# Kernel optimization log

Measured on AMD Instinct MI355X. Metric: run time of the kernel, lower is better.

## Reference

```python
import jax, jax.numpy as jnp
import numpy as np
import math

H, G, DQK, DV = 16, 4, 64, 128  # n_head, n_kv_group, qk head dim, v head dim


def _rope(t):
    # t: [B, n, T, d] -- standard rotate-half RoPE, base 10000
    B, n, T, d = t.shape
    inv = 1.0 / (10000.0 ** (jnp.arange(0, d, 2, dtype=jnp.float32) / d))  # [d/2]
    ang = jnp.arange(T, dtype=jnp.float32)[:, None] * inv[None, :]          # [T, d/2]
    cos = jnp.concatenate([jnp.cos(ang), jnp.cos(ang)], axis=-1)            # [T, d]
    sin = jnp.concatenate([jnp.sin(ang), jnp.sin(ang)], axis=-1)
    t1, t2 = jnp.split(t, 2, axis=-1)
    rot = jnp.concatenate([-t2, t1], axis=-1)
    return t * cos + rot * sin


def setup_inputs() -> dict:
    key = jax.random.key(0)
    ks = jax.random.split(key, 6)
    B, T, C = 2, 2048, 1024
    x = jax.random.normal(ks[0], (B, T, C), jnp.float32)
    Wq = jax.random.normal(ks[1], (C, H * DQK), jnp.float32) * 0.02
    Wk = jax.random.normal(ks[2], (C, G * DQK), jnp.float32) * 0.02
    Wv = jax.random.normal(ks[3], (C, G * DV), jnp.float32) * 0.02
    Wproj = jax.random.normal(ks[4], (DV, C), jnp.float32) * 0.02
    lobo = jnp.full((H,), 1.0, jnp.float32)  # flash_lobo_log_const per head
    g0 = math.log2(T * T - T)                # qk_norm_factor init from block_size
    qk_norm_factor = jnp.array([g0], dtype=jnp.float32)
    return {"x": x, "iter_num": 0, "Wq": Wq, "Wk": Wk, "Wv": Wv,
            "Wproj": Wproj, "lobo": lobo, "qk_norm_factor": qk_norm_factor}


def reference(x, iter_num, Wq, Wk, Wv, Wproj, lobo, qk_norm_factor):
    B, T, C = x.shape
    # projections (bias=False)
    q = (x @ Wq).reshape(B, T, H, DQK).transpose(0, 2, 1, 3)   # [B,H,T,dqk]
    k = (x @ Wk).reshape(B, T, G, DQK).transpose(0, 2, 1, 3)   # [B,G,T,dqk]
    v = (x @ Wv).reshape(B, T, G, DV).transpose(0, 2, 1, 3)    # [B,G,T,dv]
    # rotary embeddings on q and k
    q = _rope(q)
    k = _rope(k)
    # qk-norm
    q = q / (jnp.linalg.norm(q, axis=-1, keepdims=True) + 1e-6)
    k = k / (jnp.linalg.norm(k, axis=-1, keepdims=True) + 1e-6)
    # learned logit scale: q *= g*sqrt(d), SDPA divides by sqrt(d) -> net scale g
    q = q * (qk_norm_factor[0] * jnp.sqrt(jnp.float32(DQK)))
    # GQA broadcast (repeat_interleave over kv groups)
    rep = H // G
    k = jnp.repeat(k, rep, axis=1)   # [B,H,T,dqk]
    v = jnp.repeat(v, rep, axis=1)   # [B,H,T,dv]
    logits = jnp.einsum('bhqd,bhkd->bhqk', q, k) / jnp.sqrt(jnp.float32(DQK))
    causal = jnp.tril(jnp.ones((T, T), dtype=bool))
    logits = jnp.where(causal[None, None], logits, -jnp.inf)
    # flash-lobo: zero-valued sink key, always visible, logit = per-head bias
    sink = jnp.broadcast_to(lobo[None, :, None, None], (B, H, T, 1))
    att = jax.nn.softmax(jnp.concatenate([sink, logits], axis=-1), axis=-1)
    y = jnp.einsum('bhqk,bhkd->bhqd', att[..., 1:], v)  # sink value is zero
    y = y.sum(axis=1)                                    # head-SUM merge [B,T,dv]
    return y @ Wproj                                     # [B,T,C]
```

## Files before the change

### kernel.cpp

```cpp
#include <hip/hip_runtime.h>
#include <hip/hip_bf16.h>
#include <math.h>

#define B_ 2
#define T_ 2048
#define C_ 1024
#define H_ 16
#define G_ 4
#define DQK_ 64
#define DV_ 128
#define NQKV 1792
#define QKW 1280
#define KS2 2048

typedef __attribute__((ext_vector_type(8))) short short8;
typedef __attribute__((ext_vector_type(4))) float f32x4;
typedef unsigned short ushort_t;

__device__ inline ushort_t f2bf(float f) {
  union { float f; unsigned int u; } v; v.f = f;
  unsigned int r = (v.u + 0x7FFFu + ((v.u >> 16) & 1u)) >> 16;
  return (ushort_t)r;
}
__device__ inline float bf2f(ushort_t h) {
  union { unsigned int u; float f; } v; v.u = ((unsigned int)h) << 16;
  return v.f;
}
__device__ inline ushort_t f2bf_hw(float f) {
  unsigned int u;
  asm("v_cvt_pk_bf16_f32 %0, %1, %1" : "=v"(u) : "v"(f));
  return (ushort_t)u;
}

#define GLD_LDS16(g, l)                                              \
  __builtin_amdgcn_global_load_lds(                                  \
      (const __attribute__((address_space(1))) void*)(g),            \
      (__attribute__((address_space(3))) void*)(l), 16, 0, 0)

__global__ __launch_bounds__(256) void prep(
    const float* __restrict__ x, const float* __restrict__ Wq,
    const float* __restrict__ Wk, const float* __restrict__ Wv,
    const float* __restrict__ Wproj, ushort_t* __restrict__ xb,
    ushort_t* __restrict__ wt, ushort_t* __restrict__ wpf) {
  __shared__ float tile[64][65];
  const int bid = blockIdx.x;
  const int tid = threadIdx.x;

  if (bid < 2048) {
    int idx = bid * 256 + tid;
    int m = idx >> 7;
    int c8 = idx & 127;
    const float* src = &x[(size_t)m * 1024 + c8 * 8];
    float4 v0 = *(const float4*)&src[0];
    float4 v1 = *(const float4*)&src[4];
    float f[8] = {v0.x, v0.y, v0.z, v0.w, v1.x, v1.y, v1.z, v1.w};
    short8 hv, lv;
#pragma unroll
    for (int c = 0; c < 8; c++) {
      ushort_t h = f2bf(f[c]);
      hv[c] = (short)h;
      lv[c] = (short)f2bf(f[c] - bf2f(h));
    }
    int key = (m >> 1) & 3;
    int phys = (c8 & ~3) * 8 + ((c8 & 3) ^ key) * 8;
    ushort_t* row = xb + (size_t)m * KS2;
    *(short8*)&row[phys] = hv;
    *(short8*)&row[1024 + phys] = lv;
  } else if (bid < 2496) {
    const int wid = bid - 2048;
    const int n0 = (wid % 28) * 64;
    const int k0 = (wid / 28) * 64;

    const float* Wp; int ldw, noff;
    if (n0 < 1024)      { Wp = Wq; ldw = 1024; noff = n0; }
    else if (n0 < 1280) { Wp = Wk; ldw = 256;  noff = n0 - 1024; }
    else                { Wp = Wv; ldw = 512;  noff = n0 - 1280; }

#pragma unroll
    for (int it = 0; it < 4; it++) {
      int fi = it * 256 + tid;
      int kk = fi >> 4;
      int nc = (fi & 15) * 4;
      float4 v = *(const float4*)&Wp[(size_t)(k0 + kk) * ldw + noff + nc];
      tile[nc + 0][kk] = v.x; tile[nc + 1][kk] = v.y;
      tile[nc + 2][kk] = v.z; tile[nc + 3][kk] = v.w;
    }
    __syncthreads();
    int nn = tid >> 2, seg = tid & 3;
    int n = n0 + nn;
    int key = (n >> 1) & 3;
    ushort_t* row = wt + (size_t)n * KS2;
#pragma unroll
    for (int j = 0; j < 2; j++) {
      short8 hv;
#pragma unroll
      for (int u = 0; u < 8; u++)
        hv[u] = (short)f2bf(tile[nn][seg * 16 + j * 8 + u]);
      int c8 = (k0 >> 3) + seg * 2 + j;
      int phys = (c8 & ~3) * 8 + ((c8 & 3) ^ key) * 8;
      *(short8*)&row[phys] = hv;
    }
  } else {
    int idx = (bid - 2496) * 256 + tid;
    int n = idx & 1023;
    int kc = idx >> 10;
    short8 v;
#pragma unroll
    for (int j = 0; j < 8; j++)
      v[j] = (short)f2bf(Wproj[(size_t)(kc * 8 + j) * 1024 + n]);
    size_t off = (((size_t)(n >> 7) * 4 + (kc >> 2)) * 8 + ((n >> 4) & 7)) * 512 +
                 ((kc & 3) * 16 + (n & 15)) * 8;
    *(short8*)&wpf[off] = v;
  }
}

__global__ __launch_bounds__(256) void gemm_qkv_mfma(
    const ushort_t* __restrict__ xb, const ushort_t* __restrict__ wt,
    float* __restrict__ qkv, ushort_t* __restrict__ vf) {
  __shared__ ushort_t At[128 * 64];
  __shared__ ushort_t Bt[128 * 64];
  const int tid = threadIdx.x;
  const int wave = tid >> 6, lane = tid & 63;
  const int quad = lane >> 4, l16 = lane & 15;
  const int m0 = blockIdx.y * 128, n0 = blockIdx.x * 128;
  const int wm = (wave & 1) * 64, wn = (wave >> 1) * 64;
  const int key = (l16 >> 1) & 3;
  const int ntiles = (n0 >= 1280) ? 16 : 32;

  f32x4 acc[4][4];
#pragma unroll
  for (int i = 0; i < 4; i++)
#pragma unroll
    for (int j = 0; j < 4; j++) acc[i][j] = (f32x4){0.f, 0.f, 0.f, 0.f};

  const int rA = wave * 32 + (lane >> 3);
  const int cA = (lane & 7) * 8;
  const ushort_t* gA = xb + (size_t)(m0 + rA) * KS2 + cA;
  const ushort_t* gB = wt + (size_t)(n0 + rA) * KS2 + cA;

  for (int kt = 0; kt < ntiles; kt++) {
    const int ca = kt * 64;
    const int cb = (kt < 16 ? kt : kt - 16) * 64;
    __syncthreads();
#pragma unroll
    for (int j = 0; j < 4; j++) {
      GLD_LDS16(gA + ca + (size_t)(8 * j) * KS2, &At[(wave * 32 + 8 * j) * 64]);
      GLD_LDS16(gB + cb + (size_t)(8 * j) * KS2, &Bt[(wave * 32 + 8 * j) * 64]);
    }
    __syncthreads();

#pragma unroll
    for (int s = 0; s < 2; s++) {
      const int off = s * 32 + ((quad ^ key) * 8);
      short8 af[4], bf[4];
#pragma unroll
      for (int i = 0; i < 4; i++)
        af[i] = *(const short8*)&At[(wm + 16 * i + l16) * 64 + off];
#pragma unroll
      for (int j = 0; j < 4; j++)
        bf[j] = *(const short8*)&Bt[(wn + 16 * j + l16) * 64 + off];
#pragma unroll
      for (int i = 0; i < 4; i++)
#pragma unroll
        for (int j = 0; j < 4; j++)
          acc[i][j] = __builtin_amdgcn_mfma_f32_16x16x32_bf16(
              af[i], bf[j], acc[i][j], 0, 0, 0);
    }
  }

  if (n0 >= 1280) {
    const int g = (n0 - 1280) >> 7;
    ushort_t* vg = vf + (size_t)g * 262144;
#pragma unroll
    for (int i = 0; i < 4; i++) {
      int mbase = m0 + wm + 16 * i + quad * 4;
#pragma unroll
      for (int jn = 0; jn < 4; jn++) {
        int nv = (wn >> 4) + jn;
#pragma unroll
        for (int r = 0; r < 4; r++) {
          int m = mbase + r;
          int b = m >> 11, t = m & 2047;
          int tk = t >> 6, ks = (t >> 5) & 1, qd = (t >> 3) & 3, jj = t & 7;
          size_t off = (size_t)b * 4 * 262144 +
                       ((size_t)(tk * 16 + ks * 8 + nv) * 4 + qd) * 128 +
                       l16 * 8 + jj;
          vg[off] = f2bf(acc[i][jn][r]);
        }
      }
    }
  } else {
#pragma unroll
    for (int i = 0; i < 4; i++) {
      int m = m0 + wm + 16 * i + quad * 4;
#pragma unroll
      for (int j = 0; j < 4; j++) {
        int n = n0 + wn + 16 * j + l16;
#pragma unroll
        for (int r = 0; r < 4; r++)
          qkv[(size_t)(m + r) * QKW + n] = acc[i][j][r];
      }
    }
  }
}

__global__ __launch_bounds__(256) void rope_scatter(
    const float* __restrict__ qkv, ushort_t* __restrict__ qf,
    ushort_t* __restrict__ kf, float* __restrict__ y) {
  const int bid = blockIdx.x;
  const int tid = threadIdx.x;

  if (bid < 20480) {
    const int NQ = B_ * T_ * H_;
    int vec = bid * 4 + (tid >> 6);
    int d = tid & 63;

    size_t src; int t, b, isq; ushort_t* dstbase;
    if (vec < NQ) {
      int h = vec % H_; int bt = vec / H_;
      t = bt % T_; b = bt / T_;
      src = (size_t)bt * QKW + h * 64 + d;
      dstbase = qf + (size_t)(b * 16 + h) * 131072;
      isq = 1;
    } else {
      int vk = vec - NQ;
      int g = vk % G_; int bt = vk / G_;
      t = bt % T_; b = bt / T_;
      src = (size_t)bt * QKW + 1024 + g * 64 + d;
      dstbase = kf + (size_t)(b * 4 + g) * 131072;
      isq = 0;
    }
    float val = qkv[src];
    int i = d & 31;
    float inv = exp2f(-(float)i * 0.4152410118074239f);
    float ang = (float)t * inv;
    float sn, cs;
    __sincosf(ang, &sn, &cs);
    float partner = __shfl(val, d ^ 32, 64);
    float r = (d < 32) ? (val * cs - partner * sn) : (val * cs + partner * sn);
    float ss = r * r;
#pragma unroll
    for (int off = 32; off; off >>= 1) ss += __shfl_xor(ss, off, 64);
    r *= 1.0f / (sqrtf(ss) + 1e-6f);

    int kt = t >> 6, tt = t & 63;
    int l16v = tt & 15;
    int ks = d >> 5, quad = (d >> 3) & 3, j = d & 7;
    size_t off2;
    if (isq) {
      int wavei = tt >> 4;
      off2 = ((size_t)(kt * 8 + wavei * 2 + ks) * 4 + quad) * 128 + l16v * 8 + j;
    } else {
      int nt = tt >> 4;
      off2 = ((size_t)(kt * 8 + ks * 4 + nt) * 4 + quad) * 128 + l16v * 8 + j;
    }
    dstbase[off2] = f2bf(r);
  } else {
    int idx = (bid - 20480) * 256 + tid;
    *(float4*)&y[(size_t)idx * 4] = (float4){0.f, 0.f, 0.f, 0.f};
  }
}

__global__ __launch_bounds__(256, 4) void attn(
    const ushort_t* __restrict__ qf, const ushort_t* __restrict__ kf,
    const ushort_t* __restrict__ vf, const float* __restrict__ lobo,
    const float* __restrict__ qknf, float* __restrict__ y) {
  const int f = blockIdx.x;
  const int bh = f & 31;
  const int slot = f >> 5;
  int tq;
  if (slot < 8)       tq = 31 - slot;
  else if (slot < 16) tq = 8 + slot;
  else if (slot < 24) tq = 31 - slot;
  else                tq = slot - 24;
  const int b = bh >> 4;
  const int h = bh & 15;
  const int g = h >> 2;

  __shared__ ushort_t KV[12288];
  __shared__ ushort_t Ps[4 * 1088];

  const int tid = threadIdx.x;
  const int wave = tid >> 6, lane = tid & 63;
  const int quad = lane >> 4, l16 = lane & 15;
  ushort_t* PsW = &Ps[wave * 1088];

  short8 bones;
  {
    short bv = (l16 == 0) ? (short)0x3F80 : (short)0;
#pragma unroll
    for (int j = 0; j < 8; j++) bones[j] = bv;
  }

  const ushort_t* qbase = qf + (size_t)(b * 16 + h) * 131072 + lane * 8;
  short8 aq0 = *(const short8*)&qbase[(size_t)(tq * 8 + wave * 2 + 0) * 512];
  short8 aq1 = *(const short8*)&qbase[(size_t)(tq * 8 + wave * 2 + 1) * 512];

  f32x4 o[9];
#pragma unroll
  for (int nv = 0; nv < 9; nv++) o[nv] = (f32x4){0.f, 0.f, 0.f, 0.f};

  const float gsc = qknf[0];
  const float sinkp = __expf(lobo[h] - gsc);

  const int row = tq * 64 + wave * 16 + quad * 4;

  const ushort_t* kgl = kf + (size_t)(b * 4 + g) * 131072 + lane * 8;
  const ushort_t* vgl = vf + (size_t)(b * 4 + g) * 262144 + lane * 8;

  for (int kt = 0; kt <= tq; kt++) {
    __syncthreads();
    {
      const ushort_t* gk = kgl + (size_t)kt * 4096;
      const ushort_t* gv = vgl + (size_t)kt * 8192;
      GLD_LDS16(gk + (wave * 2 + 0) * 512, &KV[(wave * 2 + 0) * 512]);
      GLD_LDS16(gk + (wave * 2 + 1) * 512, &KV[(wave * 2 + 1) * 512]);
#pragma unroll
      for (int j = 0; j < 4; j++)
        GLD_LDS16(gv + (wave * 4 + j) * 512, &KV[4096 + (wave * 4 + j) * 512]);
    }
    __syncthreads();

    f32x4 s[4];
#pragma unroll
    for (int nt = 0; nt < 4; nt++) s[nt] = (f32x4){0.f, 0.f, 0.f, 0.f};
    {
      short8 kb[4];
#pragma unroll
      for (int u = 0; u < 4; u++)
        kb[u] = *(const short8*)&KV[u * 512 + lane * 8];
      __builtin_amdgcn_s_setprio(1);
#pragma unroll
      for (int nt = 0; nt < 4; nt++)
        s[nt] = __builtin_amdgcn_mfma_f32_16x16x32_bf16(aq0, kb[nt], s[nt], 0, 0, 0);
      __builtin_amdgcn_s_setprio(0);
#pragma unroll
      for (int u = 0; u < 4; u++)
        kb[u] = *(const short8*)&KV[(4 + u) * 512 + lane * 8];
      __builtin_amdgcn_s_setprio(1);
#pragma unroll
      for (int nt = 0; nt < 4; nt++)
        s[nt] = __builtin_amdgcn_mfma_f32_16x16x32_bf16(aq1, kb[nt], s[nt], 0, 0, 0);
      __builtin_amdgcn_s_setprio(0);
    }

    if (kt == tq) {
#pragma unroll
      for (int nt = 0; nt < 4; nt++) {
        int key = kt * 64 + l16 + nt * 16;
#pragma unroll
        for (int r = 0; r < 4; r++) {
          float pv = (key <= row + r) ? __expf(fmaf(s[nt][r], gsc, -gsc)) : 0.f;
          PsW[(quad * 4 + r) * 68 + nt * 16 + l16] = f2bf_hw(pv);
        }
      }
    } else {
#pragma unroll
      for (int nt = 0; nt < 4; nt++)
#pragma unroll
        for (int r = 0; r < 4; r++)
          PsW[(quad * 4 + r) * 68 + nt * 16 + l16] =
              f2bf_hw(__expf(fmaf(s[nt][r], gsc, -gsc)));
    }

    short8 ap0 = *(const short8*)&PsW[l16 * 68 + quad * 8];
    short8 ap1 = *(const short8*)&PsW[l16 * 68 + 32 + quad * 8];
    {
      short8 vb[4];
#pragma unroll
      for (int u = 0; u < 4; u++)
        vb[u] = *(const short8*)&KV[4096 + u * 512 + lane * 8];
      __builtin_amdgcn_s_setprio(1);
#pragma unroll
      for (int nv = 0; nv < 4; nv++)
        o[nv] = __builtin_amdgcn_mfma_f32_16x16x32_bf16(ap0, vb[nv], o[nv], 0, 0, 0);
      __builtin_amdgcn_s_setprio(0);
#pragma unroll
      for (int u = 0; u < 4; u++)
        vb[u] = *(const short8*)&KV[4096 + (4 + u) * 512 + lane * 8];
      __builtin_amdgcn_s_setprio(1);
#pragma unroll
      for (int nv = 0; nv < 4; nv++)
        o[4 + nv] = __builtin_amdgcn_mfma_f32_16x16x32_bf16(ap0, vb[nv], o[4 + nv], 0, 0, 0);
      o[8] = __builtin_amdgcn_mfma_f32_16x16x32_bf16(ap0, bones, o[8], 0, 0, 0);
      o[8] = __builtin_amdgcn_mfma_f32_16x16x32_bf16(ap1, bones, o[8], 0, 0, 0);
      __builtin_amdgcn_s_setprio(0);
#pragma unroll
      for (int u = 0; u < 4; u++)
        vb[u] = *(const short8*)&KV[4096 + (8 + u) * 512 + lane * 8];
      __builtin_amdgcn_s_setprio(1);
#pragma unroll
      for (int nv = 0; nv < 4; nv++)
        o[nv] = __builtin_amdgcn_mfma_f32_16x16x32_bf16(ap1, vb[nv], o[nv], 0, 0, 0);
      __builtin_amdgcn_s_setprio(0);
#pragma unroll
      for (int u = 0; u < 4; u++)
        vb[u] = *(const short8*)&KV[4096 + (12 + u) * 512 + lane * 8];
      __builtin_amdgcn_s_setprio(1);
#pragma unroll
      for (int nv = 0; nv < 4; nv++)
        o[4 + nv] = __builtin_amdgcn_mfma_f32_16x16x32_bf16(ap1, vb[nv], o[4 + nv], 0, 0, 0);
      __builtin_amdgcn_s_setprio(0);
    }
  }

#pragma unroll
  for (int r = 0; r < 4; r++) {
    float lm = __shfl(o[8][r], lane & 48, 64);
    float invl = 1.0f / (lm + sinkp);
    size_t gRow = (size_t)b * T_ + row + r;
#pragma unroll
    for (int nv = 0; nv < 8; nv++)
      atomicAdd(&y[gRow * 128 + nv * 16 + l16], o[nv][r] * invl);
  }
}

__global__ __launch_bounds__(256) void out_proj(
    const float* __restrict__ y, const ushort_t* __restrict__ wpf,
    float* __restrict__ out) {
  __shared__ ushort_t yl[128 * 136];
  const int tid = threadIdx.x;
  const int wave = tid >> 6, lane = tid & 63;
  const int quad = lane >> 4, l16 = lane & 15;
  const int n0 = blockIdx.x * 128, m0 = blockIdx.y * 128;
  const int wm = (wave & 1) * 64, wn = (wave >> 1) * 64;

#pragma unroll
  for (int it = 0; it < 8; it++) {
    int p = it * 256 + tid;
    int row = p >> 4, c8 = p & 15;
    const float* src = &y[(size_t)(m0 + row) * 128 + c8 * 8];
    float4 v0 = *(const float4*)&src[0];
    float4 v1 = *(const float4*)&src[4];
    float fv[8] = {v0.x, v0.y, v0.z, v0.w, v1.x, v1.y, v1.z, v1.w};
    short8 hv;
#pragma unroll
    for (int c = 0; c < 8; c++) hv[c] = (short)f2bf(fv[c]);
    *(short8*)&yl[row * 136 + c8 * 8] = hv;
  }
  __syncthreads();

  f32x4 acc[4][4];
#pragma unroll
  for (int i = 0; i < 4; i++)
#pragma unroll
    for (int j = 0; j < 4; j++) acc[i][j] = (f32x4){0.f, 0.f, 0.f, 0.f};

#pragma unroll
  for (int ks = 0; ks < 4; ks++) {
    short8 af[4], bfr[4];
#pragma unroll
    for (int i = 0; i < 4; i++)
      af[i] = *(const short8*)&yl[(wm + 16 * i + l16) * 136 + (ks * 4 + quad) * 8];
    const ushort_t* wb = wpf + (((size_t)(n0 >> 7) * 4 + ks) * 8) * 512;
#pragma unroll
    for (int j = 0; j < 4; j++)
      bfr[j] = *(const short8*)&wb[((size_t)((wn >> 4) + j)) * 512 + lane * 8];
#pragma unroll
    for (int i = 0; i < 4; i++)
#pragma unroll
      for (int j = 0; j < 4; j++)
        acc[i][j] = __builtin_amdgcn_mfma_f32_16x16x32_bf16(
            af[i], bfr[j], acc[i][j], 0, 0, 0);
  }

#pragma unroll
  for (int i = 0; i < 4; i++) {
    int m = m0 + wm + 16 * i + quad * 4;
#pragma unroll
    for (int j = 0; j < 4; j++) {
      int n = n0 + wn + 16 * j + l16;
#pragma unroll
      for (int r = 0; r < 4; r++)
        out[(size_t)(m + r) * 1024 + n] = acc[i][j][r];
    }
  }
}

extern "C" void kernel_launch(void* const* d_in, const int* in_sizes, int n_in,
                              void* d_out, int out_size, void* d_ws, size_t ws_size,
                              hipStream_t stream) {
  const float* x     = (const float*)d_in[0];
  const float* Wq    = (const float*)d_in[2];
  const float* Wk    = (const float*)d_in[3];
  const float* Wv    = (const float*)d_in[4];
  const float* Wproj = (const float*)d_in[5];
  const float* lobo  = (const float*)d_in[6];
  const float* qknf  = (const float*)d_in[7];
  float* out = (float*)d_out;

  float* qkvfull = (float*)d_ws;
  float* qkv = qkvfull;
  ushort_t* vf = (ushort_t*)(qkvfull + (size_t)B_ * T_ * QKW);
  ushort_t* xb = (ushort_t*)(qkvfull + (size_t)B_ * T_ * NQKV);
  ushort_t* wt = xb + (size_t)B_ * T_ * KS2;
  ushort_t* wpf = wt + (size_t)NQKV * KS2;
  ushort_t* qf = xb;
  ushort_t* kf = qf + (size_t)B_ * H_ * T_ * 64;
  float* y = (float*)(kf + (size_t)B_ * G_ * T_ * 64);

  prep<<<2560, 256, 0, stream>>>(x, Wq, Wk, Wv, Wproj, xb, wt, wpf);

  dim3 gg(NQKV / 128, (B_ * T_) / 128);
  gemm_qkv_mfma<<<gg, 256, 0, stream>>>(xb, wt, qkv, vf);

  rope_scatter<<<20992, 256, 0, stream>>>(qkv, qf, kf, y);

  attn<<<B_ * H_ * 32, 256, 0, stream>>>(qf, kf, vf, lobo, qknf, y);

  dim3 go(8, 32);
  out_proj<<<go, 256, 0, stream>>>(y, wpf, out);
}
```

Baseline: 214.5 us.

## Fuse RoPE and qk-norm into QKV GEMM epilogue, drop rope_scatter kernel

The QKV GEMM epilogue now applies rotary embedding and L2 normalisation in registers and writes bf16 q/k directly in the attention layout. This removes the fp32 qkv intermediate and the separate rope_scatter launch. The zeroing of y moves into the prep kernel. The epilogue relies on each wave's 64-column slice covering exactly one head, pairing accumulator columns j and j+2 for rotate-half and reducing the norm with shuffles across 16 lanes. It adds sincos work and scattered 2-byte stores to the GEMM.

```diff
diff --git a/kernel.cpp b/kernel.cpp
--- a/kernel.cpp
+++ b/kernel.cpp
@@ -10,7 +10,6 @@
 #define DQK_ 64
 #define DV_ 128
 #define NQKV 1792
-#define QKW 1280
 #define KS2 2048
 
 typedef __attribute__((ext_vector_type(8))) short short8;
@@ -41,7 +40,8 @@
     const float* __restrict__ x, const float* __restrict__ Wq,
     const float* __restrict__ Wk, const float* __restrict__ Wv,
     const float* __restrict__ Wproj, ushort_t* __restrict__ xb,
-    ushort_t* __restrict__ wt, ushort_t* __restrict__ wpf) {
+    ushort_t* __restrict__ wt, ushort_t* __restrict__ wpf,
+    float* __restrict__ y) {
   __shared__ float tile[64][65];
   const int bid = blockIdx.x;
   const int tid = threadIdx.x;
@@ -100,7 +100,7 @@
       int phys = (c8 & ~3) * 8 + ((c8 & 3) ^ key) * 8;
       *(short8*)&row[phys] = hv;
     }
-  } else {
+  } else if (bid < 2560) {
     int idx = (bid - 2496) * 256 + tid;
     int n = idx & 1023;
     int kc = idx >> 10;
@@ -111,12 +111,16 @@
     size_t off = (((size_t)(n >> 7) * 4 + (kc >> 2)) * 8 + ((n >> 4) & 7)) * 512 +
                  ((kc & 3) * 16 + (n & 15)) * 8;
     *(short8*)&wpf[off] = v;
+  } else {
+    int idx = (bid - 2560) * 256 + tid;
+    *(float4*)&y[(size_t)idx * 4] = (float4){0.f, 0.f, 0.f, 0.f};
   }
 }
 
 __global__ __launch_bounds__(256) void gemm_qkv_mfma(
     const ushort_t* __restrict__ xb, const ushort_t* __restrict__ wt,
-    float* __restrict__ qkv, ushort_t* __restrict__ vf) {
+    ushort_t* __restrict__ qf, ushort_t* __restrict__ kf,
+    ushort_t* __restrict__ vf) {
   __shared__ ushort_t At[128 * 64];
   __shared__ ushort_t Bt[128 * 64];
   const int tid = threadIdx.x;
@@ -168,9 +172,11 @@
     }
   }
 
+  const int b = m0 >> 11;
+
   if (n0 >= 1280) {
     const int g = (n0 - 1280) >> 7;
-    ushort_t* vg = vf + (size_t)g * 262144;
+    ushort_t* vg = vf + (size_t)(b * 4 + g) * 262144;
 #pragma unroll
     for (int i = 0; i < 4; i++) {
       int mbase = m0 + wm + 16 * i + quad * 4;
@@ -179,85 +185,56 @@
         int nv = (wn >> 4) + jn;
 #pragma unroll
         for (int r = 0; r < 4; r++) {
-          int m = mbase + r;
-          int b = m >> 11, t = m & 2047;
+          int t = (mbase + r) & 2047;
           int tk = t >> 6, ks = (t >> 5) & 1, qd = (t >> 3) & 3, jj = t & 7;
-          size_t off = (size_t)b * 4 * 262144 +
-                       ((size_t)(tk * 16 + ks * 8 + nv) * 4 + qd) * 128 +
+          size_t off = ((size_t)(tk * 16 + ks * 8 + nv) * 4 + qd) * 128 +
                        l16 * 8 + jj;
           vg[off] = f2bf(acc[i][jn][r]);
         }
       }
     }
   } else {
+    const int headn = n0 + wn;
+    const bool isq = headn < 1024;
+    ushort_t* dstbase = isq
+        ? qf + (size_t)(b * 16 + (headn >> 6)) * 131072
+        : kf + (size_t)(b * 4 + ((headn - 1024) >> 6)) * 131072;
+    const float c0 = 0.4152410118074239f;
+    const float inv_lo = exp2f(-(float)l16 * c0);
+    const float inv_hi = exp2f(-(float)(16 + l16) * c0);
+    const int jj = l16 & 7;
+
 #pragma unroll
     for (int i = 0; i < 4; i++) {
-      int m = m0 + wm + 16 * i + quad * 4;
-#pragma unroll
-      for (int j = 0; j < 4; j++) {
-        int n = n0 + wn + 16 * j + l16;
-#pragma unroll
-        for (int r = 0; r < 4; r++)
-          qkv[(size_t)(m + r) * QKW + n] = acc[i][j][r];
+#pragma unroll
+      for (int r = 0; r < 4; r++) {
+        int t = (m0 + wm + 16 * i + quad * 4 + r) & 2047;
+        float sn0, cs0, sn1, cs1;
+        __sincosf((float)t * inv_lo, &sn0, &cs0);
+        __sincosf((float)t * inv_hi, &sn1, &cs1);
+        float rv0 = acc[i][0][r] * cs0 - acc[i][2][r] * sn0;
+        float rv1 = acc[i][1][r] * cs1 - acc[i][3][r] * sn1;
+        float rv2 = acc[i][2][r] * cs0 + acc[i][0][r] * sn0;
+        float rv3 = acc[i][3][r] * cs1 + acc[i][1][r] * sn1;
+        float ss = rv0 * rv0 + rv1 * rv1 + rv2 * rv2 + rv3 * rv3;
+        ss += __shfl_xor(ss, 1, 64);
+        ss += __shfl_xor(ss, 2, 64);
+        ss += __shfl_xor(ss, 4, 64);
+        ss += __shfl_xor(ss, 8, 64);
+        float sc = 1.0f / (sqrtf(ss) + 1e-6f);
+        int kt8 = t >> 6, tt = t & 63;
+        int l16v = tt & 15, nt = tt >> 4;
+        float rv[4] = {rv0, rv1, rv2, rv3};
+#pragma unroll
+        for (int j = 0; j < 4; j++) {
+          int ks = j >> 1;
+          int qd = (2 * j + (l16 >> 3)) & 3;
+          size_t idx512 = isq ? (size_t)(kt8 * 8 + nt * 2 + ks)
+                              : (size_t)(kt8 * 8 + ks * 4 + nt);
+          dstbase[idx512 * 512 + qd * 128 + l16v * 8 + jj] = f2bf(rv[j] * sc);
+        }
       }
     }
-  }
-}
-
-__global__ __launch_bounds__(256) void rope_scatter(
-    const float* __restrict__ qkv, ushort_t* __restrict__ qf,
-    ushort_t* __restrict__ kf, float* __restrict__ y) {
-  const int bid = blockIdx.x;
-  const int tid = threadIdx.x;
-
-  if (bid < 20480) {
-    const int NQ = B_ * T_ * H_;
-    int vec = bid * 4 + (tid >> 6);
-    int d = tid & 63;
-
-    size_t src; int t, b, isq; ushort_t* dstbase;
-    if (vec < NQ) {
-      int h = vec % H_; int bt = vec / H_;
-      t = bt % T_; b = bt / T_;
-      src = (size_t)bt * QKW + h * 64 + d;
-      dstbase = qf + (size_t)(b * 16 + h) * 131072;
-      isq = 1;
-    } else {
-      int vk = vec - NQ;
-      int g = vk % G_; int bt = vk / G_;
-      t = bt % T_; b = bt / T_;
-      src = (size_t)bt * QKW + 1024 + g * 64 + d;
-      dstbase = kf + (size_t)(b * 4 + g) * 131072;
-      isq = 0;
-    }
-    float val = qkv[src];
-    int i = d & 31;
-    float inv = exp2f(-(float)i * 0.4152410118074239f);
-    float ang = (float)t * inv;
-    float sn, cs;
-    __sincosf(ang, &sn, &cs);
-    float partner = __shfl(val, d ^ 32, 64);
-    float r = (d < 32) ? (val * cs - partner * sn) : (val * cs + partner * sn);
-    float ss = r * r;
-#pragma unroll
-    for (int off = 32; off; off >>= 1) ss += __shfl_xor(ss, off, 64);
-    r *= 1.0f / (sqrtf(ss) + 1e-6f);
-
-    int kt = t >> 6, tt = t & 63;
-    int l16v = tt & 15;
-    int ks = d >> 5, quad = (d >> 3) & 3, j = d & 7;
-    size_t off2;
-    if (isq) {
-      int wavei = tt >> 4;
-      off2 = ((size_t)(kt * 8 + wavei * 2 + ks) * 4 + quad) * 128 + l16v * 8 + j;
-    } else {
-      int nt = tt >> 4;
-      off2 = ((size_t)(kt * 8 + ks * 4 + nt) * 4 + quad) * 128 + l16v * 8 + j;
-    }
-    dstbase[off2] = f2bf(r);
-  } else {
-    int idx = (bid - 20480) * 256 + tid;
-    *(float4*)&y[(size_t)idx * 4] = (float4){0.f, 0.f, 0.f, 0.f};
   }
 }
 
@@ -489,22 +466,18 @@
   const float* qknf  = (const float*)d_in[7];
   float* out = (float*)d_out;
 
-  float* qkvfull = (float*)d_ws;
-  float* qkv = qkvfull;
-  ushort_t* vf = (ushort_t*)(qkvfull + (size_t)B_ * T_ * QKW);
-  ushort_t* xb = (ushort_t*)(qkvfull + (size_t)B_ * T_ * NQKV);
+  ushort_t* qf = (ushort_t*)d_ws;
+  ushort_t* kf = qf + (size_t)B_ * H_ * T_ * 64;
+  ushort_t* vf = kf + (size_t)B_ * G_ * T_ * 64;
+  float* y = (float*)(vf + (size_t)B_ * G_ * T_ * 128);
+  ushort_t* xb = (ushort_t*)((float*)d_ws + (size_t)B_ * T_ * NQKV);
   ushort_t* wt = xb + (size_t)B_ * T_ * KS2;
   ushort_t* wpf = wt + (size_t)NQKV * KS2;
-  ushort_t* qf = xb;
-  ushort_t* kf = qf + (size_t)B_ * H_ * T_ * 64;
-  float* y = (float*)(kf + (size_t)B_ * G_ * T_ * 64);
-
-  prep<<<2560, 256, 0, stream>>>(x, Wq, Wk, Wv, Wproj, xb, wt, wpf);
+
+  prep<<<3072, 256, 0, stream>>>(x, Wq, Wk, Wv, Wproj, xb, wt, wpf, y);
 
   dim3 gg(NQKV / 128, (B_ * T_) / 128);
-  gemm_qkv_mfma<<<gg, 256, 0, stream>>>(xb, wt, qkv, vf);
-
-  rope_scatter<<<20992, 256, 0, stream>>>(qkv, qf, kf, y);
+  gemm_qkv_mfma<<<gg, 256, 0, stream>>>(xb, wt, qf, kf, vf);
 
   attn<<<B_ * H_ * 32, 256, 0, stream>>>(qf, kf, vf, lobo, qknf, y);
 
```

Measured after the change: 195.9 us. -8.7%, faster.
